# Performance work log

Measured on AMD Instinct MI355X. Metric: run time of the kernel, lower is better.

## Reference

```python
import jax, jax.numpy as jnp
import numpy as np

B, T, D, H, L = 128, 512, 512, 512, 2

def setup_inputs() -> dict:
    key = jax.random.key(0)
    k1, k2 = jax.random.split(key)
    x = jax.random.normal(k1, (B, T, D), dtype=jnp.float32)
    hiddens = jnp.zeros((L, 2, B, H), dtype=jnp.float32)  # [layer, (h,c), batch, hidden]
    # stacked per-layer fused-gate weights; torch Linear(in+hid, 4*hid)
    W = jax.random.normal(k2, (L, D + H, 4 * H), dtype=jnp.float32) * (1.0 / np.sqrt(D + H))
    b = jnp.zeros((L, 4 * H), dtype=jnp.float32)
    return {"x": x, "hiddens": hiddens, "W": W, "b": b}

def reference(x, hiddens, W, b):
    num_layers = W.shape[0]

    def step(hid, x_t):
        inp = x_t
        new = []
        for l in range(num_layers):
            h, c = hid[l, 0], hid[l, 1]
            gates = jnp.concatenate([inp, h], axis=-1) @ W[l] + b[l]  # [B, 4H]
            i, f, g, o = jnp.split(gates, 4, axis=-1)
            i = jax.nn.sigmoid(i)
            f = jax.nn.sigmoid(f)
            g = jnp.tanh(g)
            o = jax.nn.sigmoid(o)
            c_t = f * c + i * g
            h_t = o * jnp.tanh(c_t)
            new.append(jnp.stack([h_t, c_t], axis=0))
            inp = h_t
        hid = jnp.stack(new, axis=0)
        return hid, inp  # emit top-layer h per timestep

    hiddens_final, outs = jax.lax.scan(step, hiddens, jnp.swapaxes(x, 0, 1))
    outputs = jnp.swapaxes(outs, 0, 1)  # [B, T, H]
    return outputs, hiddens_final
```

## Files before the change

kernel.cpp:

```cpp
#include <hip/hip_runtime.h>
#include <stdint.h>

typedef __attribute__((ext_vector_type(4))) int   i32x4;
typedef __attribute__((ext_vector_type(8))) short bf16x8;
typedef __attribute__((ext_vector_type(4))) float f32x4;

#define DEV static __device__ __forceinline__

constexpr int  kB = 128, kT = 512, kD = 512, kH = 512;
constexpr int  kGC = 2048;
constexpr int  ROWS = 32;
constexpr int  NG = 4;
constexpr int  NJ = 32;
constexpr int  NTHREADS = 512;
constexpr size_t SLOT_ELEMS = (size_t)kB * kH;
constexpr size_t WIMG_ELEMS = (size_t)2 * NJ * 4 * 32 * 512;
constexpr size_t WIMG_BYTES = WIMG_ELEMS * 2;
constexpr int  RFULL = kT + 1;
constexpr int  FLAG_STRIDE = 128;
constexpr size_t FLAG_TOTAL = (size_t)2 * NG * kT * FLAG_STRIDE;

DEV ushort f2bf(float f) {
  uint32_t u = __float_as_uint(f);
  u += 0x7fff + ((u >> 16) & 1);
  return (ushort)(u >> 16);
}
DEV int pk2(float a, float b) { return (int)((uint32_t)f2bf(a) | ((uint32_t)f2bf(b) << 16)); }
DEV float sigf(float v)  { return 1.f / (1.f + __expf(-v)); }
DEV float tanhf_(float v){ return 1.f - 2.f / (__expf(2.f * v) + 1.f); }

DEV uint64_t ald64(const uint64_t* p) {
  return __hip_atomic_load(p, __ATOMIC_RELAXED, __HIP_MEMORY_SCOPE_AGENT);
}

DEV void poll32(const uint8_t* fb) {
  const uint64_t* p = reinterpret_cast<const uint64_t*>(fb);
  constexpr uint64_t ONE = 0x0101010101010101ull;
  for (;;) {
    uint64_t a = ald64(p) & ald64(p + 1) & ald64(p + 2) & ald64(p + 3);
    if (a == ONE) return;
    __builtin_amdgcn_s_sleep(1);
  }
}

__global__ void prep_w(const float* __restrict__ W, ushort* __restrict__ wimg) {
  uint32_t idx = blockIdx.x * 256u + threadIdx.x;
  int e = idx & 7, lane = (idx >> 3) & 63, ks = (idx >> 9) & 31;
  int G = (idx >> 14) & 3, j = (idx >> 16) & 31, l = (idx >> 21) & 1;
  int k = ks * 32 + ((lane >> 4) << 3) + e;
  int c = G * 512 + j * 16 + (lane & 15);
  wimg[idx] = f2bf(W[(size_t)l * 1024 * 2048 + (size_t)k * 2048 + c]);
}

__global__ void prep_init(const float* __restrict__ hiddens, ushort* __restrict__ r0, ushort* __restrict__ r1) {
  uint32_t idx = blockIdx.x * 256u + threadIdx.x;
  int l = idx >> 16; uint32_t r = idx & 65535u;
  ushort v = f2bf(hiddens[(size_t)(l * 2 + 0) * 65536 + r]);
  (l ? r1 : r0)[r] = v;
}

DEV void stage_h(ushort* Ab, const ushort* rbase, int g, int tid) {
  #pragma unroll
  for (int p = 0; p < 4; ++p) {
    int o = (tid + p * NTHREADS) * 16, row = o >> 10, kb = o & 1023;
    i32x4 v = *reinterpret_cast<const i32x4*>(rbase + (size_t)(g * ROWS + row) * kH + (kb >> 1));
    *reinterpret_cast<i32x4*>(reinterpret_cast<char*>(Ab) + ((row * 1024 + kb) ^ ((row & 7) << 4))) = v;
  }
}

DEV int gsw(int r, int c) { return r * 16 + (c ^ ((((r) >> 2) & 3) << 2)); }

__launch_bounds__(NTHREADS, 1)
__global__ void lstm_v5(const float* __restrict__ x, const float* __restrict__ hiddens,
                        const float* __restrict__ bias, const ushort* __restrict__ wimg,
                        ushort* __restrict__ ring0, ushort* __restrict__ ring1,
                        uint8_t* __restrict__ flags, float* __restrict__ out) {
  __shared__ ushort AbufX[ROWS * 512];
  __shared__ ushort AbufH[ROWS * 512];
  __shared__ float  gbuf[2][4][ROWS * 16];

  const int tid  = threadIdx.x;
  const int lane = tid & 63;
  const int wv   = tid >> 6;
  const int kq   = wv >> 2;
  const int Gp   = (wv >> 1) & 1;
  const int rf   = wv & 1;
  const int j    = blockIdx.x & 31;
  const int g    = (blockIdx.x >> 5) & 3;
  const int l    = blockIdx.x >> 7;

  __threadfence();

  i32x4 wrA[16], wrB[16];
  {
    const int GA = 2 * Gp, GB = 2 * Gp + 1;
    const ushort* baseA = wimg + (((size_t)(l * NJ + j) * 4 + GA) * 32) * 512 + lane * 8;
    const ushort* baseB = wimg + (((size_t)(l * NJ + j) * 4 + GB) * 32) * 512 + lane * 8;
    #pragma unroll
    for (int s = 0; s < 8; ++s) {
      wrA[s]     = *reinterpret_cast<const i32x4*>(baseA + (kq * 8 + s) * 512);
      wrA[8 + s] = *reinterpret_cast<const i32x4*>(baseA + (16 + kq * 8 + s) * 512);
      wrB[s]     = *reinterpret_cast<const i32x4*>(baseB + (kq * 8 + s) * 512);
      wrB[8 + s] = *reinterpret_cast<const i32x4*>(baseB + (16 + kq * 8 + s) * 512);
    }
  }
  const int urow = tid >> 4, ucol = tid & 15;
  const float b0 = bias[l * kGC + 0 * 512 + j * 16 + ucol];
  const float b1 = bias[l * kGC + 1 * 512 + j * 16 + ucol];
  const float b2 = bias[l * kGC + 2 * 512 + j * 16 + ucol];
  const float b3 = bias[l * kGC + 3 * 512 + j * 16 + ucol];
  float creg = hiddens[((size_t)(l * 2 + 1) * kB + (g * ROWS + urow)) * kH + j * 16 + ucol];

  ushort* rrec = l ? ring1 : ring0;
  uint8_t* myflags = flags + (size_t)(l * NG + g) * kT * FLAG_STRIDE;
  const uint8_t* xflags = flags + (size_t)g * kT * FLAG_STRIDE;

  const int arow  = rf * 16 + (lane & 15);
  const int koff  = (lane >> 4) << 3;
  const int abase = arow * 1024;
  const int aswz  = (arow & 7) << 4;
  const int uswz  = gsw(urow, ucol);

  f32x4 xr[8];
  if (l == 0) {
    #pragma unroll
    for (int p = 0; p < 4; ++p) {
      int o = (tid + p * NTHREADS) * 16, row = o >> 10, kb = o & 1023;
      const float* src = x + ((size_t)(g * ROWS + row) * kT + 0) * kD + (kb >> 1);
      xr[2 * p]     = *reinterpret_cast<const f32x4*>(src);
      xr[2 * p + 1] = *reinterpret_cast<const f32x4*>(src + 4);
    }
  }

  for (int t = 0; t < kT; ++t) {
    if (l == 0) {
      #pragma unroll
      for (int p = 0; p < 4; ++p) {
        int o = (tid + p * NTHREADS) * 16, row = o >> 10, kb = o & 1023;
        i32x4 v;
        v[0] = pk2(xr[2 * p][0], xr[2 * p][1]);         v[1] = pk2(xr[2 * p][2], xr[2 * p][3]);
        v[2] = pk2(xr[2 * p + 1][0], xr[2 * p + 1][1]); v[3] = pk2(xr[2 * p + 1][2], xr[2 * p + 1][3]);
        *reinterpret_cast<i32x4*>(reinterpret_cast<char*>(AbufX) + ((row * 1024 + kb) ^ ((row & 7) << 4))) = v;
      }
    } else {
      poll32(xflags + (size_t)t * FLAG_STRIDE);
      stage_h(AbufX, ring0 + (size_t)(t + 1) * SLOT_ELEMS, g, tid);
    }
    __syncthreads();

    if (l == 0 && t + 1 < kT) {
      #pragma unroll
      for (int p = 0; p < 4; ++p) {
        int o = (tid + p * NTHREADS) * 16, row = o >> 10, kb = o & 1023;
        const float* src = x + ((size_t)(g * ROWS + row) * kT + (t + 1)) * kD + (kb >> 1);
        xr[2 * p]     = *reinterpret_cast<const f32x4*>(src);
        xr[2 * p + 1] = *reinterpret_cast<const f32x4*>(src + 4);
      }
    }

    f32x4 accA = {}, accB = {};
    #pragma unroll
    for (int s = 0; s < 8; ++s) {
      int ks = kq * 8 + s;
      int off = (abase + ((ks * 32 + koff) << 1)) ^ aswz;
      i32x4 av = *reinterpret_cast<const i32x4*>(reinterpret_cast<const char*>(AbufX) + off);
      accA = __builtin_amdgcn_mfma_f32_16x16x32_bf16(
               *reinterpret_cast<bf16x8*>(&av), *reinterpret_cast<bf16x8*>(&wrA[s]), accA, 0, 0, 0);
      accB = __builtin_amdgcn_mfma_f32_16x16x32_bf16(
               *reinterpret_cast<bf16x8*>(&av), *reinterpret_cast<bf16x8*>(&wrB[s]), accB, 0, 0, 0);
    }

    if (t > 0) poll32(myflags + (size_t)(t - 1) * FLAG_STRIDE);
    stage_h(AbufH, rrec + (size_t)t * SLOT_ELEMS, g, tid);
    __syncthreads();

    #pragma unroll
    for (int s = 0; s < 8; ++s) {
      int ks = kq * 8 + s;
      int off = (abase + ((ks * 32 + koff) << 1)) ^ aswz;
      i32x4 av = *reinterpret_cast<const i32x4*>(reinterpret_cast<const char*>(AbufH) + off);
      accA = __builtin_amdgcn_mfma_f32_16x16x32_bf16(
               *reinterpret_cast<bf16x8*>(&av), *reinterpret_cast<bf16x8*>(&wrA[8 + s]), accA, 0, 0, 0);
      accB = __builtin_amdgcn_mfma_f32_16x16x32_bf16(
               *reinterpret_cast<bf16x8*>(&av), *reinterpret_cast<bf16x8*>(&wrB[8 + s]), accB, 0, 0, 0);
    }

    #pragma unroll
    for (int q = 0; q < 4; ++q) {
      int r = rf * 16 + ((lane >> 4) << 2) + q, c = lane & 15;
      int idx = gsw(r, c);
      gbuf[kq][2 * Gp][idx]     = accA[q];
      gbuf[kq][2 * Gp + 1][idx] = accB[q];
    }
    __syncthreads();

    float hh;
    {
      float iv = sigf  (gbuf[0][0][uswz] + gbuf[1][0][uswz] + b0);
      float fv = sigf  (gbuf[0][1][uswz] + gbuf[1][1][uswz] + b1);
      float gv = tanhf_(gbuf[0][2][uswz] + gbuf[1][2][uswz] + b2);
      float ov = sigf  (gbuf[0][3][uswz] + gbuf[1][3][uswz] + b3);
      creg = fv * creg + iv * gv;
      hh = ov * tanhf_(creg);
      uint32_t me    = f2bf(hh);
      uint32_t other = (uint32_t)__shfl_xor((int)me, 1);
      if (!(ucol & 1)) {
        uint32_t pkv = me | (other << 16);
        uint32_t* dst = (uint32_t*)(rrec + (size_t)(t + 1) * SLOT_ELEMS
                                    + (size_t)(g * ROWS + urow) * kH + j * 16 + ucol);
        __hip_atomic_store(dst, pkv, __ATOMIC_RELAXED, __HIP_MEMORY_SCOPE_AGENT);
      }
    }
    asm volatile("s_waitcnt vmcnt(0)" ::: "memory");
    __syncthreads();
    if (tid == 0)
      __hip_atomic_store(myflags + (size_t)t * FLAG_STRIDE + j, (uint8_t)1,
                         __ATOMIC_RELAXED, __HIP_MEMORY_SCOPE_AGENT);

    {
      int b = g * ROWS + urow;
      if (l == 1) out[((size_t)b * kT + t) * kH + j * 16 + ucol] = hh;
      if (t == kT - 1) {
        size_t hb = (size_t)kB * kT * kH;
        out[hb + ((size_t)(l * 2 + 0) * kB + b) * kH + j * 16 + ucol] = hh;
        out[hb + ((size_t)(l * 2 + 1) * kB + b) * kH + j * 16 + ucol] = creg;
      }
    }
  }
}


template<bool BIG>
DEV void stage_ring(ushort* Abuf_, const ushort* rbase, int g, int tid) {
  #pragma unroll
  for (int p = 0; p < 4; ++p) {
    int o = (tid + p * NTHREADS) * 16;
    int row = o >> 10, kb = o & 1023;
    const ushort* src = rbase + (size_t)(g * ROWS + row) * kH + (kb >> 1);
    i32x4 v;
    if (BIG) {
      v = *reinterpret_cast<const i32x4*>(src);
    } else {
      uint64_t lo = __hip_atomic_load((const uint64_t*)src,       __ATOMIC_RELAXED, __HIP_MEMORY_SCOPE_AGENT);
      uint64_t hi = __hip_atomic_load((const uint64_t*)(src + 4), __ATOMIC_RELAXED, __HIP_MEMORY_SCOPE_AGENT);
      v[0] = (int)(uint32_t)lo; v[1] = (int)(uint32_t)(lo >> 32);
      v[2] = (int)(uint32_t)hi; v[3] = (int)(uint32_t)(hi >> 32);
    }
    *reinterpret_cast<i32x4*>(reinterpret_cast<char*>(Abuf_) + ((row * 1024 + kb) ^ ((row & 7) << 4))) = v;
  }
}

template<bool BIG>
__launch_bounds__(NTHREADS, 2)
__global__ void lstm_main(const float* __restrict__ x, const float* __restrict__ hiddens,
                          const float* __restrict__ bias, const ushort* __restrict__ wimg,
                          ushort* __restrict__ ring0, ushort* __restrict__ ring1,
                          int* __restrict__ cnt, int* __restrict__ cons0,
                          float* __restrict__ out, int R0, int R1) {
  __shared__ ushort Abuf[ROWS * 512];
  __shared__ float  gbuf[4][ROWS][16];
  __shared__ float  cbuf[ROWS][16];
  __shared__ float  hbuf[ROWS][16];

  const int tid  = threadIdx.x;
  const int lane = tid & 63;
  const int wv   = tid >> 6;
  const int G    = wv & 3;
  const int rf   = wv >> 2;
  const int j    = blockIdx.x & 31;
  const int g    = (blockIdx.x >> 5) & 3;
  const int l    = blockIdx.x >> 7;

  __threadfence();

  i32x4 wr[32];
  {
    const ushort* base = wimg + (((size_t)(l * NJ + j) * 4 + G) * 32) * 512 + lane * 8;
    #pragma unroll
    for (int ks = 0; ks < 32; ++ks)
      wr[ks] = *reinterpret_cast<const i32x4*>(base + ks * 512);
  }
  const float bval = bias[l * kGC + G * 512 + j * 16 + (lane & 15)];
  {
    int row = tid >> 4, col = tid & 15;
    cbuf[row][col] = hiddens[((size_t)(l * 2 + 1) * kB + (g * ROWS + row)) * kH + j * 16 + col];
  }
  int* mycnt = cnt + (l * NG + g) * kT;
  int* c0cnt = cnt + g * kT;
  ushort* rrec = l ? ring1 : ring0;
  const int Rrec = l ? R1 : R0;

  const int arow  = rf * 16 + (lane & 15);
  const int koff  = (lane >> 4) << 3;
  const int abase = arow * 1024;
  const int aswz  = (arow & 7) << 4;

  __syncthreads();

  for (int t = 0; t < kT; ++t) {
    if (l == 1) {
      if (tid == 0) {
        while (__hip_atomic_load(&c0cnt[t], __ATOMIC_RELAXED, __HIP_MEMORY_SCOPE_AGENT) < NJ)
          __builtin_amdgcn_s_sleep(2);
      }
      __syncthreads();
      stage_ring<BIG>(Abuf, ring0 + (size_t)((t + 1) % R0) * SLOT_ELEMS, g, tid);
    } else {
      #pragma unroll
      for (int p = 0; p < 4; ++p) {
        int o = (tid + p * NTHREADS) * 16;
        int row = o >> 10, kb = o & 1023;
        const float* src = x + ((size_t)(g * ROWS + row) * kT + t) * kD + (kb >> 1);
        f32x4 f0 = *reinterpret_cast<const f32x4*>(src);
        f32x4 f1 = *reinterpret_cast<const f32x4*>(src + 4);
        i32x4 v;
        v[0] = pk2(f0[0], f0[1]); v[1] = pk2(f0[2], f0[3]);
        v[2] = pk2(f1[0], f1[1]); v[3] = pk2(f1[2], f1[3]);
        *reinterpret_cast<i32x4*>(reinterpret_cast<char*>(Abuf) + ((row * 1024 + kb) ^ ((row & 7) << 4))) = v;
      }
    }
    __syncthreads();
    if (!BIG && l == 1 && tid == 0)
      __hip_atomic_fetch_add(&cons0[g * kT + t], 1, __ATOMIC_RELAXED, __HIP_MEMORY_SCOPE_AGENT);

    f32x4 acc = {};
    #pragma unroll
    for (int ks = 0; ks < 16; ++ks) {
      int off = (abase + ((ks * 32 + koff) << 1)) ^ aswz;
      i32x4 av = *reinterpret_cast<const i32x4*>(reinterpret_cast<const char*>(Abuf) + off);
      acc = __builtin_amdgcn_mfma_f32_16x16x32_bf16(
              *reinterpret_cast<bf16x8*>(&av), *reinterpret_cast<bf16x8*>(&wr[ks]), acc, 0, 0, 0);
    }
    __syncthreads();

    if (t > 0) {
      if (tid == 0) {
        while (__hip_atomic_load(&mycnt[t - 1], __ATOMIC_RELAXED, __HIP_MEMORY_SCOPE_AGENT) < NJ)
          __builtin_amdgcn_s_sleep(2);
        if (!BIG && l == 0 && t >= R0) {
          while (__hip_atomic_load(&cons0[g * kT + (t - R0)], __ATOMIC_RELAXED, __HIP_MEMORY_SCOPE_AGENT) < NJ)
            __builtin_amdgcn_s_sleep(2);
        }
      }
      __syncthreads();
    }
    stage_ring<BIG>(Abuf, rrec + (size_t)(t % Rrec) * SLOT_ELEMS, g, tid);
    __syncthreads();

    #pragma unroll
    for (int ks = 0; ks < 16; ++ks) {
      int off = (abase + ((ks * 32 + koff) << 1)) ^ aswz;
      i32x4 av = *reinterpret_cast<const i32x4*>(reinterpret_cast<const char*>(Abuf) + off);
      acc = __builtin_amdgcn_mfma_f32_16x16x32_bf16(
              *reinterpret_cast<bf16x8*>(&av), *reinterpret_cast<bf16x8*>(&wr[16 + ks]), acc, 0, 0, 0);
    }

    #pragma unroll
    for (int q = 0; q < 4; ++q) {
      float v2 = acc[q] + bval;
      v2 = (G == 2) ? tanhf_(v2) : sigf(v2);
      gbuf[G][rf * 16 + ((lane >> 4) << 2) + q][lane & 15] = v2;
    }
    __syncthreads();

    {
      int row = tid >> 4, col = tid & 15;
      float iv = gbuf[0][row][col], fv = gbuf[1][row][col];
      float gv = gbuf[2][row][col], ov = gbuf[3][row][col];
      float cc = fv * cbuf[row][col] + iv * gv;
      cbuf[row][col] = cc;
      float hh = ov * tanhf_(cc);
      hbuf[row][col] = hh;
      int b = g * ROWS + row;
      if (l == 1) out[((size_t)b * kT + t) * kH + j * 16 + col] = hh;
      if (t == kT - 1) {
        size_t hb = (size_t)kB * kT * kH;
        out[hb + ((size_t)(l * 2 + 0) * kB + b) * kH + j * 16 + col] = hh;
        out[hb + ((size_t)(l * 2 + 1) * kB + b) * kH + j * 16 + col] = cc;
      }
    }
    __syncthreads();

    if (tid < 256) {
      int row = tid >> 3, cp = tid & 7;
      uint32_t pkv = (uint32_t)f2bf(hbuf[row][2 * cp]) | ((uint32_t)f2bf(hbuf[row][2 * cp + 1]) << 16);
      uint32_t* dst = (uint32_t*)(rrec + (size_t)((t + 1) % Rrec) * SLOT_ELEMS
                                  + (size_t)(g * ROWS + row) * kH + j * 16 + 2 * cp);
      __hip_atomic_store(dst, pkv, __ATOMIC_RELAXED, __HIP_MEMORY_SCOPE_AGENT);
    }
    asm volatile("s_waitcnt vmcnt(0)" ::: "memory");
    __syncthreads();
    if (tid == 0)
      __hip_atomic_fetch_add(&mycnt[t], 1, __ATOMIC_RELAXED, __HIP_MEMORY_SCOPE_AGENT);
  }
}

extern "C" void kernel_launch(void* const* d_in, const int* in_sizes, int n_in,
                              void* d_out, int out_size, void* d_ws, size_t ws_size,
                              hipStream_t stream) {
  const float* x  = (const float*)d_in[0];
  const float* hd = (const float*)d_in[1];
  const float* W  = (const float*)d_in[2];
  const float* b  = (const float*)d_in[3];
  float* out = (float*)d_out;

  char* ws = (char*)d_ws;
  ushort* wimg = (ushort*)ws;
  uint8_t* flags = (uint8_t*)(ws + WIMG_BYTES);
  int* cnt  = (int*)(ws + WIMG_BYTES + FLAG_TOTAL);
  int* cons = (int*)(ws + WIMG_BYTES + FLAG_TOTAL + 16384);
  size_t ringoff = WIMG_BYTES + FLAG_TOTAL + 32768;
  size_t avail = ws_size > ringoff ? ws_size - ringoff : 0;
  long rmax = (long)(avail / (2 * SLOT_ELEMS * 2));
  int R = (rmax >= RFULL) ? RFULL : (rmax >= 16 ? 16 : (rmax >= 2 ? (int)rmax : 2));
  ushort* ring0 = (ushort*)(ws + ringoff);
  ushort* ring1 = ring0 + (size_t)R * SLOT_ELEMS;

  prep_w<<<(int)(WIMG_ELEMS / 256), 256, 0, stream>>>(W, wimg);
  prep_init<<<(2 * kB * kH) / 256, 256, 0, stream>>>(hd, ring0, ring1);
  if (R == RFULL) {
    hipMemsetAsync(flags, 0, FLAG_TOTAL, stream);
    lstm_v5<<<256, NTHREADS, 0, stream>>>(x, hd, b, wimg, ring0, ring1, flags, out);
  } else {
    hipMemsetAsync(ws + WIMG_BYTES + FLAG_TOTAL, 0, 32768, stream);
    lstm_main<false><<<256, NTHREADS, 0, stream>>>(x, hd, b, wimg, ring0, ring1, cnt, cons, out, R, R);
  }
}
```

Measured before the change: 2.063 ms.

## Replace end-of-step barrier with LDS counter and speculatively prefetch ring slots

The end-of-step __syncthreads is replaced by an LDS atomic counter. Only wave 0 spins on it before publishing the block's flag, so other waves can move on to the next timestep. After each step, every thread checks whether the next h slot (counting its own block as done) and, for layer 1, the next layer-0 output slot are already flagged. If so it loads them into registers early, skipping the blocking poll and hiding global load latency behind compute. The speculative own-block assumption and the removed barrier add risk of reading ring data that other waves of the same block have not yet stored, and they cost extra registers and flag reads.

```diff
diff --git a/kernel.cpp b/kernel.cpp
--- a/kernel.cpp
+++ b/kernel.cpp
@@ -19,6 +19,7 @@
 constexpr int  RFULL = kT + 1;
 constexpr int  FLAG_STRIDE = 128;
 constexpr size_t FLAG_TOTAL = (size_t)2 * NG * kT * FLAG_STRIDE;
+constexpr uint64_t ONE8 = 0x0101010101010101ull;
 
 DEV ushort f2bf(float f) {
   uint32_t u = __float_as_uint(f);
@@ -35,12 +36,22 @@
 
 DEV void poll32(const uint8_t* fb) {
   const uint64_t* p = reinterpret_cast<const uint64_t*>(fb);
-  constexpr uint64_t ONE = 0x0101010101010101ull;
   for (;;) {
     uint64_t a = ald64(p) & ald64(p + 1) & ald64(p + 2) & ald64(p + 3);
-    if (a == ONE) return;
+    if (a == ONE8) return;
     __builtin_amdgcn_s_sleep(1);
   }
+}
+DEV bool chk32_own(const uint8_t* fb, int j) {
+  const uint64_t* p = reinterpret_cast<const uint64_t*>(fb);
+  uint64_t own = 0xFFull << ((j & 7) * 8);
+  uint64_t w0 = ald64(p), w1 = ald64(p + 1), w2 = ald64(p + 2), w3 = ald64(p + 3);
+  if (j < 8) w0 |= own; else if (j < 16) w1 |= own; else if (j < 24) w2 |= own; else w3 |= own;
+  return (w0 & w1 & w2 & w3) == ONE8;
+}
+DEV bool chk32(const uint8_t* fb) {
+  const uint64_t* p = reinterpret_cast<const uint64_t*>(fb);
+  return (ald64(p) & ald64(p + 1) & ald64(p + 2) & ald64(p + 3)) == ONE8;
 }
 
 __global__ void prep_w(const float* __restrict__ W, ushort* __restrict__ wimg) {
@@ -67,17 +78,32 @@
     *reinterpret_cast<i32x4*>(reinterpret_cast<char*>(Ab) + ((row * 1024 + kb) ^ ((row & 7) << 4))) = v;
   }
 }
+DEV void ldslot(i32x4* r, const ushort* rbase, int g, int tid) {
+  #pragma unroll
+  for (int p = 0; p < 4; ++p) {
+    int o = (tid + p * NTHREADS) * 16, row = o >> 10, kb = o & 1023;
+    r[p] = *reinterpret_cast<const i32x4*>(rbase + (size_t)(g * ROWS + row) * kH + (kb >> 1));
+  }
+}
+DEV void wrslot(ushort* Ab, const i32x4* r, int tid) {
+  #pragma unroll
+  for (int p = 0; p < 4; ++p) {
+    int o = (tid + p * NTHREADS) * 16, row = o >> 10, kb = o & 1023;
+    *reinterpret_cast<i32x4*>(reinterpret_cast<char*>(Ab) + ((row * 1024 + kb) ^ ((row & 7) << 4))) = r[p];
+  }
+}
 
 DEV int gsw(int r, int c) { return r * 16 + (c ^ ((((r) >> 2) & 3) << 2)); }
 
 __launch_bounds__(NTHREADS, 1)
-__global__ void lstm_v5(const float* __restrict__ x, const float* __restrict__ hiddens,
+__global__ void lstm_v6(const float* __restrict__ x, const float* __restrict__ hiddens,
                         const float* __restrict__ bias, const ushort* __restrict__ wimg,
                         ushort* __restrict__ ring0, ushort* __restrict__ ring1,
                         uint8_t* __restrict__ flags, float* __restrict__ out) {
   __shared__ ushort AbufX[ROWS * 512];
   __shared__ ushort AbufH[ROWS * 512];
   __shared__ float  gbuf[2][4][ROWS * 16];
+  __shared__ int    dcnt[2];
 
   const int tid  = threadIdx.x;
   const int lane = tid & 63;
@@ -91,6 +117,8 @@
 
   __threadfence();
 
+  if (tid == 0) { dcnt[0] = 0; dcnt[1] = 0; }
+
   i32x4 wrA[16], wrB[16];
   {
     const int GA = 2 * Gp, GB = 2 * Gp + 1;
@@ -122,6 +150,11 @@
   const int uswz  = gsw(urow, ucol);
 
   f32x4 xr[8];
+  i32x4 xregi[4];
+  i32x4 hreg[4];
+  bool hok = true;
+  bool xok = false;
+
   if (l == 0) {
     #pragma unroll
     for (int p = 0; p < 4; ++p) {
@@ -131,8 +164,12 @@
       xr[2 * p + 1] = *reinterpret_cast<const f32x4*>(src + 4);
     }
   }
+  __syncthreads();
 
   for (int t = 0; t < kT; ++t) {
+    if (!hok) poll32(myflags + (size_t)(t - 1) * FLAG_STRIDE);
+    ldslot(hreg, rrec + (size_t)t * SLOT_ELEMS, g, tid);
+
     if (l == 0) {
       #pragma unroll
       for (int p = 0; p < 4; ++p) {
@@ -143,8 +180,12 @@
         *reinterpret_cast<i32x4*>(reinterpret_cast<char*>(AbufX) + ((row * 1024 + kb) ^ ((row & 7) << 4))) = v;
       }
     } else {
-      poll32(xflags + (size_t)t * FLAG_STRIDE);
-      stage_h(AbufX, ring0 + (size_t)(t + 1) * SLOT_ELEMS, g, tid);
+      if (xok) {
+        wrslot(AbufX, xregi, tid);
+      } else {
+        poll32(xflags + (size_t)t * FLAG_STRIDE);
+        stage_h(AbufX, ring0 + (size_t)(t + 1) * SLOT_ELEMS, g, tid);
+      }
     }
     __syncthreads();
 
@@ -170,8 +211,7 @@
                *reinterpret_cast<bf16x8*>(&av), *reinterpret_cast<bf16x8*>(&wrB[s]), accB, 0, 0, 0);
     }
 
-    if (t > 0) poll32(myflags + (size_t)(t - 1) * FLAG_STRIDE);
-    stage_h(AbufH, rrec + (size_t)t * SLOT_ELEMS, g, tid);
+    wrslot(AbufH, hreg, tid);
     __syncthreads();
 
     #pragma unroll
@@ -211,11 +251,25 @@
         __hip_atomic_store(dst, pkv, __ATOMIC_RELAXED, __HIP_MEMORY_SCOPE_AGENT);
       }
     }
+
     asm volatile("s_waitcnt vmcnt(0)" ::: "memory");
-    __syncthreads();
-    if (tid == 0)
+    if (lane == 0)
+      __hip_atomic_fetch_add(&dcnt[t & 1], 1, __ATOMIC_RELAXED, __HIP_MEMORY_SCOPE_WORKGROUP);
+    if (wv == 0 && lane == 0) {
+      while (__hip_atomic_load(&dcnt[t & 1], __ATOMIC_RELAXED, __HIP_MEMORY_SCOPE_WORKGROUP) < 8)
+        __builtin_amdgcn_s_sleep(0);
+      __hip_atomic_store(&dcnt[t & 1], 0, __ATOMIC_RELAXED, __HIP_MEMORY_SCOPE_WORKGROUP);
       __hip_atomic_store(myflags + (size_t)t * FLAG_STRIDE + j, (uint8_t)1,
                          __ATOMIC_RELAXED, __HIP_MEMORY_SCOPE_AGENT);
+    }
+
+    if (t + 1 < kT) {
+      hok = chk32_own(myflags + (size_t)t * FLAG_STRIDE, j);
+      if (l == 1) {
+        xok = chk32(xflags + (size_t)(t + 1) * FLAG_STRIDE);
+        if (xok) ldslot(xregi, ring0 + (size_t)(t + 2) * SLOT_ELEMS, g, tid);
+      }
+    }
 
     {
       int b = g * ROWS + urow;
@@ -420,7 +474,7 @@
   prep_init<<<(2 * kB * kH) / 256, 256, 0, stream>>>(hd, ring0, ring1);
   if (R == RFULL) {
     hipMemsetAsync(flags, 0, FLAG_TOTAL, stream);
-    lstm_v5<<<256, NTHREADS, 0, stream>>>(x, hd, b, wimg, ring0, ring1, flags, out);
+    lstm_v6<<<256, NTHREADS, 0, stream>>>(x, hd, b, wimg, ring0, ring1, flags, out);
   } else {
     hipMemsetAsync(ws + WIMG_BYTES + FLAG_TOTAL, 0, 32768, stream);
     lstm_main<false><<<256, NTHREADS, 0, stream>>>(x, hd, b, wimg, ring0, ring1, cnt, cons, out, R, R);
```

After: 3.678 ms. 1.78x slower.

## Stage per-wave K-quarter of hidden state and poll only matching flags, dropping barriers

Applied to the files above, without the earlier changes.

Each wave now stages into shared memory only the rows and K-range it reads itself (its rf half and kq quarter). It also polls only the 16 producer flags covering that K-quarter instead of all 32. This removes two block-wide __syncthreads per timestep, so waves can start their MFMAs as soon as their own slice of h is ready, which shortens the serial recurrent critical path. In exchange each wave loads twice as many vectors per stage, and correctness depends on no wave reading shared-memory data staged by another wave.

```diff
diff --git a/kernel.cpp b/kernel.cpp
--- a/kernel.cpp
+++ b/kernel.cpp
@@ -19,6 +19,7 @@
 constexpr int  RFULL = kT + 1;
 constexpr int  FLAG_STRIDE = 128;
 constexpr size_t FLAG_TOTAL = (size_t)2 * NG * kT * FLAG_STRIDE;
+constexpr uint64_t ONE8 = 0x0101010101010101ull;
 
 DEV ushort f2bf(float f) {
   uint32_t u = __float_as_uint(f);
@@ -35,10 +36,16 @@
 
 DEV void poll32(const uint8_t* fb) {
   const uint64_t* p = reinterpret_cast<const uint64_t*>(fb);
-  constexpr uint64_t ONE = 0x0101010101010101ull;
   for (;;) {
     uint64_t a = ald64(p) & ald64(p + 1) & ald64(p + 2) & ald64(p + 3);
-    if (a == ONE) return;
+    if (a == ONE8) return;
+    __builtin_amdgcn_s_sleep(1);
+  }
+}
+DEV void poll16(const uint8_t* fb) {
+  const uint64_t* p = reinterpret_cast<const uint64_t*>(fb);
+  for (;;) {
+    if ((ald64(p) & ald64(p + 1)) == ONE8) return;
     __builtin_amdgcn_s_sleep(1);
   }
 }
@@ -59,10 +66,12 @@
   (l ? r1 : r0)[r] = v;
 }
 
-DEV void stage_h(ushort* Ab, const ushort* rbase, int g, int tid) {
+DEV void stage_q(ushort* Ab, const ushort* rbase, int g, int rf, int kq, int lane) {
   #pragma unroll
-  for (int p = 0; p < 4; ++p) {
-    int o = (tid + p * NTHREADS) * 16, row = o >> 10, kb = o & 1023;
+  for (int p = 0; p < 8; ++p) {
+    int c = lane + p * 64;
+    int row = rf * 16 + (c >> 5);
+    int kb  = kq * 512 + (c & 31) * 16;
     i32x4 v = *reinterpret_cast<const i32x4*>(rbase + (size_t)(g * ROWS + row) * kH + (kb >> 1));
     *reinterpret_cast<i32x4*>(reinterpret_cast<char*>(Ab) + ((row * 1024 + kb) ^ ((row & 7) << 4))) = v;
   }
@@ -71,10 +80,10 @@
 DEV int gsw(int r, int c) { return r * 16 + (c ^ ((((r) >> 2) & 3) << 2)); }
 
 __launch_bounds__(NTHREADS, 1)
-__global__ void lstm_v5(const float* __restrict__ x, const float* __restrict__ hiddens,
-                        const float* __restrict__ bias, const ushort* __restrict__ wimg,
-                        ushort* __restrict__ ring0, ushort* __restrict__ ring1,
-                        uint8_t* __restrict__ flags, float* __restrict__ out) {
+__global__ void lstm_v10(const float* __restrict__ x, const float* __restrict__ hiddens,
+                         const float* __restrict__ bias, const ushort* __restrict__ wimg,
+                         ushort* __restrict__ ring0, ushort* __restrict__ ring1,
+                         uint8_t* __restrict__ flags, float* __restrict__ out) {
   __shared__ ushort AbufX[ROWS * 512];
   __shared__ ushort AbufH[ROWS * 512];
   __shared__ float  gbuf[2][4][ROWS * 16];
@@ -142,20 +151,19 @@
         v[2] = pk2(xr[2 * p + 1][0], xr[2 * p + 1][1]); v[3] = pk2(xr[2 * p + 1][2], xr[2 * p + 1][3]);
         *reinterpret_cast<i32x4*>(reinterpret_cast<char*>(AbufX) + ((row * 1024 + kb) ^ ((row & 7) << 4))) = v;
       }
+      __syncthreads();
+      if (t + 1 < kT) {
+        #pragma unroll
+        for (int p = 0; p < 4; ++p) {
+          int o = (tid + p * NTHREADS) * 16, row = o >> 10, kb = o & 1023;
+          const float* src = x + ((size_t)(g * ROWS + row) * kT + (t + 1)) * kD + (kb >> 1);
+          xr[2 * p]     = *reinterpret_cast<const f32x4*>(src);
+          xr[2 * p + 1] = *reinterpret_cast<const f32x4*>(src + 4);
+        }
+      }
     } else {
-      poll32(xflags + (size_t)t * FLAG_STRIDE);
-      stage_h(AbufX, ring0 + (size_t)(t + 1) * SLOT_ELEMS, g, tid);
-    }
-    __syncthreads();
-
-    if (l == 0 && t + 1 < kT) {
-      #pragma unroll
-      for (int p = 0; p < 4; ++p) {
-        int o = (tid + p * NTHREADS) * 16, row = o >> 10, kb = o & 1023;
-        const float* src = x + ((size_t)(g * ROWS + row) * kT + (t + 1)) * kD + (kb >> 1);
-        xr[2 * p]     = *reinterpret_cast<const f32x4*>(src);
-        xr[2 * p + 1] = *reinterpret_cast<const f32x4*>(src + 4);
-      }
+      poll16(xflags + (size_t)t * FLAG_STRIDE + kq * 16);
+      stage_q(AbufX, ring0 + (size_t)(t + 1) * SLOT_ELEMS, g, rf, kq, lane);
     }
 
     f32x4 accA = {}, accB = {};
@@ -170,9 +178,8 @@
                *reinterpret_cast<bf16x8*>(&av), *reinterpret_cast<bf16x8*>(&wrB[s]), accB, 0, 0, 0);
     }
 
-    if (t > 0) poll32(myflags + (size_t)(t - 1) * FLAG_STRIDE);
-    stage_h(AbufH, rrec + (size_t)t * SLOT_ELEMS, g, tid);
-    __syncthreads();
+    if (t > 0) poll16(myflags + (size_t)(t - 1) * FLAG_STRIDE + kq * 16);
+    stage_q(AbufH, rrec + (size_t)t * SLOT_ELEMS, g, rf, kq, lane);
 
     #pragma unroll
     for (int s = 0; s < 8; ++s) {
@@ -420,7 +427,7 @@
   prep_init<<<(2 * kB * kH) / 256, 256, 0, stream>>>(hd, ring0, ring1);
   if (R == RFULL) {
     hipMemsetAsync(flags, 0, FLAG_TOTAL, stream);
-    lstm_v5<<<256, NTHREADS, 0, stream>>>(x, hd, b, wimg, ring0, ring1, flags, out);
+    lstm_v10<<<256, NTHREADS, 0, stream>>>(x, hd, b, wimg, ring0, ring1, flags, out);
   } else {
     hipMemsetAsync(ws + WIMG_BYTES + FLAG_TOTAL, 0, 32768, stream);
     lstm_main<false><<<256, NTHREADS, 0, stream>>>(x, hd, b, wimg, ring0, ring1, cnt, cons, out, R, R);
```

After: 2.519 ms. 22.1% more time.
